# Kernel tuning notes

Measured on AMD Instinct MI355X. Metric: run time of the kernel, lower is better.

## Reference

```python
import jax, jax.numpy as jnp
import numpy as np

N_NODES = 100000
N_EDGES = 400000
D_FEAT = 128
HIDDEN = 64
BETA = 1.0  # temperature default in concrete_sample


def setup_inputs() -> dict:
    key = jax.random.key(0)
    k = jax.random.split(key, 6)
    embed = jax.random.normal(k[0], (N_NODES, D_FEAT), dtype=jnp.float32)
    # elayers: Linear(4*F, 64) -> ReLU -> Linear(64, 1)
    W1 = jax.random.normal(k[1], (4 * D_FEAT, HIDDEN), dtype=jnp.float32) * (1.0 / np.sqrt(4 * D_FEAT))
    b1 = jnp.zeros((HIDDEN,), dtype=jnp.float32)
    W2 = jax.random.normal(k[2], (HIDDEN, 1), dtype=jnp.float32) * (1.0 / np.sqrt(HIDDEN))
    b2 = jnp.zeros((1,), dtype=jnp.float32)
    # per-edge uniform noise, as in torch.rand(w.size()); keep away from {0,1}
    noise = jax.random.uniform(k[3], (N_EDGES,), dtype=jnp.float32, minval=1e-6, maxval=1.0 - 1e-6)
    col = jax.random.randint(k[4], (N_EDGES,), 0, N_NODES, dtype=jnp.int64 if jax.config.jax_enable_x64 else jnp.int32)
    row = jax.random.randint(k[5], (N_EDGES,), 0, N_NODES, dtype=jnp.int64 if jax.config.jax_enable_x64 else jnp.int32)
    return {"embed": embed, "W1": W1, "b1": b1, "W2": W2, "b2": b2,
            "noise": noise, "col": col, "row": row, "src_idx": 0, "dst_idx": 1}


def reference(embed, W1, b1, W2, b2, noise, col, row, src_idx, dst_idx):
    E = col.shape[0]
    F = embed.shape[1]
    # gather per-edge endpoint embeddings + broadcast explained src/dst embeddings
    col_emb = embed[col]                                    # [E, F]
    row_emb = embed[row]                                    # [E, F]
    src_emb = jnp.broadcast_to(embed[src_idx], (E, F))       # [E, F]
    dst_emb = jnp.broadcast_to(embed[dst_idx], (E, F))       # [E, F]
    emb = jnp.concatenate([col_emb, row_emb, src_emb, dst_emb], axis=-1)  # [E, 4F]
    # elayers MLP
    h = jax.nn.relu(emb @ W1 + b1)                          # [E, 64]
    w = (h @ W2 + b2).reshape(-1)                           # [E]
    # concrete_sample (training=True, sample_bias=0): logit(noise) + w, sigmoid
    gate_inputs = (jnp.log(noise) - jnp.log1p(-noise) + w) / BETA
    values = jax.nn.sigmoid(gate_inputs)                    # [E] edge mask
    return values
```

## Files before the change

### kernel.cpp

```cpp
#include <hip/hip_runtime.h>
#include <hip/hip_bf16.h>


typedef __bf16 bf16x8 __attribute__((ext_vector_type(8)));
typedef float  f32x16 __attribute__((ext_vector_type(16)));
typedef unsigned short u16;

#define WSTR 264
#define Z16 {0.f,0.f,0.f,0.f,0.f,0.f,0.f,0.f,0.f,0.f,0.f,0.f,0.f,0.f,0.f,0.f}

__device__ __forceinline__ unsigned bfbits(float f){
  unsigned u = __builtin_bit_cast(unsigned, f);
  return (u + 0x7fffu + ((u >> 16) & 1u)) >> 16;
}
__device__ __forceinline__ unsigned pk2(float a, float b){
  return bfbits(a) | (bfbits(b) << 16);
}
__device__ __forceinline__ float bflo(unsigned u){ return __builtin_bit_cast(float, u << 16); }
__device__ __forceinline__ float bfhi(unsigned u){ return __builtin_bit_cast(float, u & 0xffff0000u); }

__global__ __launch_bounds__(256, 3) void fg_kernel(
    const float* __restrict__ embed, const float* __restrict__ W1,
    const float* __restrict__ b1, const int* __restrict__ srcp,
    const int* __restrict__ dstp, u16* __restrict__ F, u16* __restrict__ G, int NN)
{
  __shared__ __align__(16) u16 sW[64 * WSTR];
  __shared__ float sC[64];
  __shared__ float sRed[256];
  int tid = threadIdx.x;

  #pragma unroll
  for (int i = 0; i < 16; ++i){
    int idx = i * 256 + tid;
    int k = idx >> 4, q = idx & 15;
    float4 v = *(const float4*)(W1 + k * 64 + q * 4);
    sW[(4*q+0) * WSTR + k] = (u16)bfbits(v.x);
    sW[(4*q+1) * WSTR + k] = (u16)bfbits(v.y);
    sW[(4*q+2) * WSTR + k] = (u16)bfbits(v.z);
    sW[(4*q+3) * WSTR + k] = (u16)bfbits(v.w);
  }
  {
    int h = tid & 63, part = tid >> 6;
    int si = srcp[0], di = dstp[0];
    const float* se  = embed + (size_t)si * 128 + part * 32;
    const float* de  = embed + (size_t)di * 128 + part * 32;
    const float* w1s = W1 + (256 + part * 32) * 64 + h;
    const float* w1d = W1 + (384 + part * 32) * 64 + h;
    float acc = 0.f;
    #pragma unroll 8
    for (int k = 0; k < 32; ++k){
      acc += se[k] * w1s[k * 64];
      acc += de[k] * w1d[k * 64];
    }
    sRed[tid] = acc;
  }
  __syncthreads();
  if (tid < 64) sC[tid] = b1[tid] + sRed[tid] + sRed[64+tid] + sRed[128+tid] + sRed[192+tid];
  __syncthreads();

  int lane = tid & 63, wave = tid >> 6;
  int nl = lane & 31, h5 = lane >> 5;
  int tile = blockIdx.x * 128 + wave * 32;
  if (tile >= NN) return;
  const float* erow = embed + (size_t)(tile + nl) * 128;
  f32x16 aF0 = Z16, aF1 = Z16, aG0 = Z16, aG1 = Z16;
  const u16* sw0 = sW + nl * WSTR;
  const u16* sw1 = sW + (32 + nl) * WSTR;
  #pragma unroll
  for (int s = 0; s < 8; ++s){
    int ko = s * 16 + h5 * 8;
    float4 x = *(const float4*)(erow + ko);
    float4 y = *(const float4*)(erow + ko + 4);
    uint4 u; u.x = pk2(x.x,x.y); u.y = pk2(x.z,x.w); u.z = pk2(y.x,y.y); u.w = pk2(y.z,y.w);
    bf16x8 a = __builtin_bit_cast(bf16x8, u);
    bf16x8 bF0 = *(const bf16x8*)(sw0 + ko);
    bf16x8 bF1 = *(const bf16x8*)(sw1 + ko);
    bf16x8 bG0 = *(const bf16x8*)(sw0 + 128 + ko);
    bf16x8 bG1 = *(const bf16x8*)(sw1 + 128 + ko);
    aF0 = __builtin_amdgcn_mfma_f32_32x32x16_bf16(a, bF0, aF0, 0, 0, 0);
    aF1 = __builtin_amdgcn_mfma_f32_32x32x16_bf16(a, bF1, aF1, 0, 0, 0);
    aG0 = __builtin_amdgcn_mfma_f32_32x32x16_bf16(a, bG0, aG0, 0, 0, 0);
    aG1 = __builtin_amdgcn_mfma_f32_32x32x16_bf16(a, bG1, aG1, 0, 0, 0);
  }
  float cv0 = sC[nl], cv1 = sC[32 + nl];
  #pragma unroll
  for (int r = 0; r < 16; ++r){
    int node = tile + (r & 3) + 8 * (r >> 2) + 4 * h5;
    u16* fr = F + (size_t)node * 64 + nl;
    u16* gr = G + (size_t)node * 64 + nl;
    fr[0]  = (u16)bfbits(aF0[r] + cv0);
    fr[32] = (u16)bfbits(aF1[r] + cv1);
    gr[0]  = (u16)bfbits(aG0[r]);
    gr[32] = (u16)bfbits(aG1[r]);
  }
}

__global__ __launch_bounds__(256, 8) void edge_kernel(
    const u16* __restrict__ F, const u16* __restrict__ G,
    const float* __restrict__ W2, const float* __restrict__ b2,
    const float* __restrict__ noise, const int* __restrict__ col,
    const int* __restrict__ row, float* __restrict__ out, int E)
{
  int tid = threadIdx.x;
  int lane = tid & 63, wave = tid >> 6;
  int j = lane & 7, grp = lane >> 3;
  int e0 = blockIdx.x * 32 + wave * 8;
  if (e0 >= E) return;
  int e = e0 + grp; if (e >= E) e = E - 1;
  int ci = col[e], ri = row[e];
  uint4 fv = ((const uint4*)(F + (size_t)ci * 64))[j];
  uint4 gv = ((const uint4*)(G + (size_t)ri * 64))[j];
  float4 w2a = ((const float4*)W2)[2 * j];
  float4 w2b = ((const float4*)W2)[2 * j + 1];
  float p = 0.f, h;
  h = fmaxf(bflo(fv.x) + bflo(gv.x), 0.f); p += h * w2a.x;
  h = fmaxf(bfhi(fv.x) + bfhi(gv.x), 0.f); p += h * w2a.y;
  h = fmaxf(bflo(fv.y) + bflo(gv.y), 0.f); p += h * w2a.z;
  h = fmaxf(bfhi(fv.y) + bfhi(gv.y), 0.f); p += h * w2a.w;
  h = fmaxf(bflo(fv.z) + bflo(gv.z), 0.f); p += h * w2b.x;
  h = fmaxf(bfhi(fv.z) + bfhi(gv.z), 0.f); p += h * w2b.y;
  h = fmaxf(bflo(fv.w) + bflo(gv.w), 0.f); p += h * w2b.z;
  h = fmaxf(bfhi(fv.w) + bfhi(gv.w), 0.f); p += h * w2b.w;
  p += __shfl_xor(p, 1, 64);
  p += __shfl_xor(p, 2, 64);
  p += __shfl_xor(p, 4, 64);
  if (j == 0 && e0 + grp < E){
    float ns = noise[e];
    float g = logf(ns) - log1pf(-ns) + p + b2[0];
    out[e] = 1.f / (1.f + expf(-g));
  }
}

__global__ void naive_kernel(const float* __restrict__ embed, const float* __restrict__ W1,
    const float* __restrict__ b1, const float* __restrict__ W2, const float* __restrict__ b2,
    const float* __restrict__ noise, const int* __restrict__ col, const int* __restrict__ row,
    const int* __restrict__ srcp, const int* __restrict__ dstp, float* __restrict__ out, int E)
{
  int e = blockIdx.x * 256 + threadIdx.x;
  if (e >= E) return;
  int ci = col[e], ri = row[e], si = srcp[0], di = dstp[0];
  const float* ce = embed + (size_t)ci * 128;
  const float* re = embed + (size_t)ri * 128;
  const float* se = embed + (size_t)si * 128;
  const float* de = embed + (size_t)di * 128;
  float w = b2[0];
  for (int jj = 0; jj < 64; ++jj){
    float hh = b1[jj];
    for (int k = 0; k < 128; ++k){
      hh += ce[k] * W1[k * 64 + jj] + re[k] * W1[(128 + k) * 64 + jj]
          + se[k] * W1[(256 + k) * 64 + jj] + de[k] * W1[(384 + k) * 64 + jj];
    }
    w += fmaxf(hh, 0.f) * W2[jj];
  }
  float ns = noise[e];
  float g = logf(ns) - log1pf(-ns) + w;
  out[e] = 1.f / (1.f + expf(-g));
}

extern "C" void kernel_launch(void* const* d_in, const int* in_sizes, int n_in,
                              void* d_out, int out_size, void* d_ws, size_t ws_size,
                              hipStream_t stream)
{
  const float* embed = (const float*)d_in[0];
  const float* W1    = (const float*)d_in[1];
  const float* b1    = (const float*)d_in[2];
  const float* W2    = (const float*)d_in[3];
  const float* b2    = (const float*)d_in[4];
  const float* noise = (const float*)d_in[5];
  const int*   col   = (const int*)d_in[6];
  const int*   rowp  = (const int*)d_in[7];
  const int*   srcp  = (const int*)d_in[8];
  const int*   dstp  = (const int*)d_in[9];
  const int E  = in_sizes[5];
  const int NN = in_sizes[0] / 128;
  float* out = (float*)d_out;

  const size_t fBytes = (size_t)NN * 64 * sizeof(u16);
  if (ws_size >= 2 * fBytes){
    u16* F = (u16*)d_ws;
    u16* G = (u16*)((char*)d_ws + fBytes);
    fg_kernel<<<(NN + 127) / 128, 256, 0, stream>>>(embed, W1, b1, srcp, dstp, F, G, NN);
    edge_kernel<<<(E + 31) / 32, 256, 0, stream>>>(F, G, W2, b2, noise, col, rowp, out, E);
  } else {
    naive_kernel<<<(E + 255) / 256, 256, 0, stream>>>(embed, W1, b1, W2, b2, noise,
                                                      col, rowp, srcp, dstp, out, E);
  }
}
```

Measured before the change: 136.8 us.

## Software-pipeline edge gathers in persistent waves and pack paired bf16 stores

After: 138.9 us. About the same (+1.5%).

```diff
diff --git a/kernel.cpp b/kernel.cpp
--- a/kernel.cpp
+++ b/kernel.cpp
@@ -83,20 +83,33 @@
     aG1 = __builtin_amdgcn_mfma_f32_32x32x16_bf16(a, bG1, aG1, 0, 0, 0);
   }
   float cv0 = sC[nl], cv1 = sC[32 + nl];
+  int lo = lane & 1;
+  int nlp = nl & ~1;
   #pragma unroll
-  for (int r = 0; r < 16; ++r){
-    int node = tile + (r & 3) + 8 * (r >> 2) + 4 * h5;
-    u16* fr = F + (size_t)node * 64 + nl;
-    u16* gr = G + (size_t)node * 64 + nl;
-    fr[0]  = (u16)bfbits(aF0[r] + cv0);
-    fr[32] = (u16)bfbits(aF1[r] + cv1);
-    gr[0]  = (u16)bfbits(aG0[r]);
-    gr[32] = (u16)bfbits(aG1[r]);
+  for (int r = 0; r < 16; r += 2){
+    int ra = r + lo;
+    int node = tile + (ra & 3) + 8 * (ra >> 2) + 4 * h5;
+    u16* fr = F + (size_t)node * 64 + nlp;
+    u16* gr = G + (size_t)node * 64 + nlp;
+    float f0a = aF0[r]   + cv0;
+    float f0b = aF0[r+1] + cv0;
+    float f0an = __shfl_xor(f0a, 1), f0bn = __shfl_xor(f0b, 1);
+    *(unsigned*)(fr)      = lo ? pk2(f0bn, f0b) : pk2(f0a, f0an);
+    float f1a = aF1[r]   + cv1;
+    float f1b = aF1[r+1] + cv1;
+    float f1an = __shfl_xor(f1a, 1), f1bn = __shfl_xor(f1b, 1);
+    *(unsigned*)(fr + 32) = lo ? pk2(f1bn, f1b) : pk2(f1a, f1an);
+    float g0a = aG0[r], g0b = aG0[r+1];
+    float g0an = __shfl_xor(g0a, 1), g0bn = __shfl_xor(g0b, 1);
+    *(unsigned*)(gr)      = lo ? pk2(g0bn, g0b) : pk2(g0a, g0an);
+    float g1a = aG1[r], g1b = aG1[r+1];
+    float g1an = __shfl_xor(g1a, 1), g1bn = __shfl_xor(g1b, 1);
+    *(unsigned*)(gr + 32) = lo ? pk2(g1bn, g1b) : pk2(g1a, g1an);
   }
 }
 
 __global__ __launch_bounds__(256, 8) void edge_kernel(
-    const u16* __restrict__ F, const u16* __restrict__ G,
+    const u16* __restrict__ Ft, const u16* __restrict__ Gt,
     const float* __restrict__ W2, const float* __restrict__ b2,
     const float* __restrict__ noise, const int* __restrict__ col,
     const int* __restrict__ row, float* __restrict__ out, int E)
@@ -104,31 +117,61 @@
   int tid = threadIdx.x;
   int lane = tid & 63, wave = tid >> 6;
   int j = lane & 7, grp = lane >> 3;
-  int e0 = blockIdx.x * 32 + wave * 8;
-  if (e0 >= E) return;
-  int e = e0 + grp; if (e >= E) e = E - 1;
-  int ci = col[e], ri = row[e];
-  uint4 fv = ((const uint4*)(F + (size_t)ci * 64))[j];
-  uint4 gv = ((const uint4*)(G + (size_t)ri * 64))[j];
+  int gw = blockIdx.x * 4 + wave;
+  int NW = gridDim.x * 4;
+  int nOct = (E + 7) >> 3;
+  int per  = (nOct + NW - 1) / NW;
+  int o0 = gw * per;
+  if (o0 >= nOct) return;
+  int o1 = o0 + per; if (o1 > nOct) o1 = nOct;
+
   float4 w2a = ((const float4*)W2)[2 * j];
   float4 w2b = ((const float4*)W2)[2 * j + 1];
-  float p = 0.f, h;
-  h = fmaxf(bflo(fv.x) + bflo(gv.x), 0.f); p += h * w2a.x;
-  h = fmaxf(bfhi(fv.x) + bfhi(gv.x), 0.f); p += h * w2a.y;
-  h = fmaxf(bflo(fv.y) + bflo(gv.y), 0.f); p += h * w2a.z;
-  h = fmaxf(bfhi(fv.y) + bfhi(gv.y), 0.f); p += h * w2a.w;
-  h = fmaxf(bflo(fv.z) + bflo(gv.z), 0.f); p += h * w2b.x;
-  h = fmaxf(bfhi(fv.z) + bfhi(gv.z), 0.f); p += h * w2b.y;
-  h = fmaxf(bflo(fv.w) + bflo(gv.w), 0.f); p += h * w2b.z;
-  h = fmaxf(bfhi(fv.w) + bfhi(gv.w), 0.f); p += h * w2b.w;
-  p += __shfl_xor(p, 1, 64);
-  p += __shfl_xor(p, 2, 64);
-  p += __shfl_xor(p, 4, 64);
-  if (j == 0 && e0 + grp < E){
-    float ns = noise[e];
-    float g = logf(ns) - log1pf(-ns) + p + b2[0];
-    out[e] = 1.f / (1.f + expf(-g));
-  }
+  float bb = b2[0];
+
+#define LOADIDX(oo, ci, ri, ns) { int e_ = (oo) * 8 + grp; if (e_ >= E) e_ = E - 1; \
+    ci = col[e_]; ri = row[e_]; ns = noise[e_]; }
+#define GATHER(ci, ri, fv, gv) { \
+    fv = ((const uint4*)(Ft + (size_t)(ci) * 64))[j]; \
+    gv = ((const uint4*)(Gt + (size_t)(ri) * 64))[j]; }
+#define COMPUTE(oo, fv, gv, ns) { \
+    float p = 0.f, h; \
+    h = fmaxf(bflo(fv.x) + bflo(gv.x), 0.f); p += h * w2a.x; \
+    h = fmaxf(bfhi(fv.x) + bfhi(gv.x), 0.f); p += h * w2a.y; \
+    h = fmaxf(bflo(fv.y) + bflo(gv.y), 0.f); p += h * w2a.z; \
+    h = fmaxf(bfhi(fv.y) + bfhi(gv.y), 0.f); p += h * w2a.w; \
+    h = fmaxf(bflo(fv.z) + bflo(gv.z), 0.f); p += h * w2b.x; \
+    h = fmaxf(bfhi(fv.z) + bfhi(gv.z), 0.f); p += h * w2b.y; \
+    h = fmaxf(bflo(fv.w) + bflo(gv.w), 0.f); p += h * w2b.z; \
+    h = fmaxf(bfhi(fv.w) + bfhi(gv.w), 0.f); p += h * w2b.w; \
+    p += __shfl_xor(p, 1, 64); \
+    p += __shfl_xor(p, 2, 64); \
+    p += __shfl_xor(p, 4, 64); \
+    int e_ = (oo) * 8 + grp; \
+    if (j == 0 && e_ < E){ \
+      float g_ = logf(ns) - log1pf(-ns) + p + bb; \
+      out[e_] = 1.f / (1.f + expf(-g_)); \
+    } }
+
+  int o = o0;
+  int ciA, riA; float nsA; LOADIDX(o,     ciA, riA, nsA);
+  int ciB, riB; float nsB; LOADIDX(o + 1, ciB, riB, nsB);
+  uint4 fC, gC; GATHER(ciA, riA, fC, gC);
+  float nsC = nsA;
+
+  #pragma unroll 2
+  for (; o + 1 < o1; ++o){
+    int ciN, riN; float nsN; LOADIDX(o + 2, ciN, riN, nsN);
+    uint4 fN, gN; GATHER(ciB, riB, fN, gN);
+    COMPUTE(o, fC, gC, nsC);
+    fC = fN; gC = gN; nsC = nsB;
+    ciB = ciN; riB = riN; nsB = nsN;
+  }
+  COMPUTE(o, fC, gC, nsC);
+
+#undef LOADIDX
+#undef GATHER
+#undef COMPUTE
 }
 
 __global__ void naive_kernel(const float* __restrict__ embed, const float* __restrict__ W1,
@@ -180,7 +223,7 @@
     u16* F = (u16*)d_ws;
     u16* G = (u16*)((char*)d_ws + fBytes);
     fg_kernel<<<(NN + 127) / 128, 256, 0, stream>>>(embed, W1, b1, srcp, dstp, F, G, NN);
-    edge_kernel<<<(E + 31) / 32, 256, 0, stream>>>(F, G, W2, b2, noise, col, rowp, out, E);
+    edge_kernel<<<2048, 256, 0, stream>>>(F, G, W2, b2, noise, col, rowp, out, E);
   } else {
     naive_kernel<<<(E + 255) / 256, 256, 0, stream>>>(embed, W1, b1, W2, b2, noise,
                                                       col, rowp, srcp, dstp, out, E);
```
